# Kernel tuning notes

Measured on AMD Instinct MI355X. Metric: run time of the kernel, lower is better.

Reference implementation:

```python
import jax, jax.numpy as jnp
import numpy as np

N_NODES = 50000
N_EDGES = 300000
D = 256
N_RELS = 500


def setup_inputs() -> dict:
    key = jax.random.key(0)
    ks = jax.random.split(key, 12)
    s = 1.0 / np.sqrt(D)  # keep activations O(1) through the dense transforms
    return {
        "h": jax.random.normal(ks[0], (N_NODES, D), dtype=jnp.float32),
        "prev_h": jax.random.normal(ks[1], (N_NODES, D), dtype=jnp.float32),
        "emb_rel": jax.random.normal(ks[2], (N_RELS, D), dtype=jnp.float32),
        "norm": jax.random.uniform(ks[3], (N_NODES, 1), dtype=jnp.float32),
        "weight_neighbor": jax.random.normal(ks[4], (D, D), dtype=jnp.float32) * s,
        "loop_weight": jax.random.normal(ks[5], (D, D), dtype=jnp.float32) * s,
        "evolve_loop_weight": jax.random.normal(ks[6], (D, D), dtype=jnp.float32) * s,
        "skip_connect_weight": jax.random.normal(ks[7], (D, D), dtype=jnp.float32) * s,
        "skip_connect_bias": jnp.zeros((D,), dtype=jnp.float32),
        "src": jax.random.randint(ks[8], (N_EDGES,), 0, N_NODES),
        "dst": jax.random.randint(ks[9], (N_EDGES,), 0, N_NODES),
        "etype": jax.random.randint(ks[10], (N_EDGES,), 0, N_RELS),
    }


def reference(h, prev_h, emb_rel, norm, weight_neighbor, loop_weight,
              evolve_loop_weight, skip_connect_weight, skip_connect_bias,
              src, dst, etype):
    n_nodes = h.shape[0]
    # msg_func: per-edge gather of src features + relation embedding, dense transform
    msg = (h[src] + emb_rel[etype]) @ weight_neighbor          # [E, D]
    # fn.sum: segment-sum messages into destination nodes
    agg = jax.ops.segment_sum(msg, dst, num_segments=n_nodes)  # [N, D]
    # apply_func: multiply by per-node norm
    agg = agg * norm
    # self-loop: loop_weight where in_degree > 0, evolve_loop_weight otherwise
    in_deg = jax.ops.segment_sum(jnp.ones_like(dst), dst, num_segments=n_nodes)
    has_in = (in_deg > 0)[:, None]
    loop_message = jnp.where(has_in, h @ loop_weight, h @ evolve_loop_weight)
    # skip connection gate
    skip_weight = jax.nn.sigmoid(prev_h @ skip_connect_weight + skip_connect_bias)
    node_repr = skip_weight * (agg + loop_message) + (1.0 - skip_weight) * prev_h
    return jax.nn.relu(node_repr)
```

## Files before the change

### kernel.cpp

```cpp
#include <hip/hip_runtime.h>
#include <cstdint>
#include <cstddef>

#define N_NODES 50000
#define N_EDGES 300000
#define DIM     256
#define KTOT    768
#define N_RELS  500
#define XW      768

#define SCAN_BLK  256
#define SCAN_NBLK ((N_NODES + SCAN_BLK - 1) / SCAN_BLK)

#define CONV_ELEMS ((2 * N_NODES + N_RELS) * DIM)
#define CONV_BLKS  ((CONV_ELEMS / 8 + 255) / 256)
#define HIST_BLKS  ((N_EDGES + 255) / 256)

typedef unsigned short u16;
typedef __attribute__((ext_vector_type(8))) short short8v;
typedef __attribute__((ext_vector_type(4))) float float4v;

static __device__ __forceinline__ u16 f2bf(float f) {
    union { float f; unsigned u; } v; v.f = f;
    unsigned u = v.u;
    unsigned r = u + 0x7FFFu + ((u >> 16) & 1u);
    return (u16)(r >> 16);
}
static __device__ __forceinline__ float bf2f(u16 b) {
    union { unsigned u; float f; } v; v.u = ((unsigned)b) << 16; return v.f;
}

static __device__ __forceinline__ void gld16(const void* g, u16* l) {
    __builtin_amdgcn_global_load_lds(
        (const __attribute__((address_space(1))) unsigned int*)g,
        (__attribute__((address_space(3))) unsigned int*)l,
        16, 0, 0);
}

__global__ void prep_kernel(const float* __restrict__ h, const float* __restrict__ prev_h,
                            const float* __restrict__ emb,
                            const float* __restrict__ Wn, const float* __restrict__ Wl,
                            const float* __restrict__ Wsc, const int* __restrict__ dstv,
                            u16* __restrict__ Xcat, u16* __restrict__ embb,
                            u16* __restrict__ Wt, int* __restrict__ deg) {
    int b = blockIdx.x;
    if (b < CONV_BLKS) {
        int i = b * 256 + threadIdx.x;
        int e0 = i * 8;
        if (e0 >= CONV_ELEMS) return;
        const float* s; u16* d;
        if (e0 < N_NODES * DIM) {
            int n = e0 >> 8, c = e0 & 255;
            s = h + e0; d = Xcat + (size_t)n * XW + 256 + c;
        } else if (e0 < 2 * N_NODES * DIM) {
            int o = e0 - N_NODES * DIM;
            int n = o >> 8, c = o & 255;
            s = prev_h + o; d = Xcat + (size_t)n * XW + 512 + c;
        } else {
            int o = e0 - 2 * N_NODES * DIM;
            s = emb + o; d = embb + o;
        }
        float4 a = *(const float4*)(s);
        float4 c2 = *(const float4*)(s + 4);
        u16 o8[8] = { f2bf(a.x), f2bf(a.y), f2bf(a.z), f2bf(a.w),
                      f2bf(c2.x), f2bf(c2.y), f2bf(c2.z), f2bf(c2.w) };
        *(uint4*)d = *(const uint4*)o8;
    } else if (b < CONV_BLKS + KTOT) {
        int k = b - CONV_BLKS;
        int dd = threadIdx.x;
        const float* W = (k < 256) ? Wn : ((k < 512) ? Wl : Wsc);
        Wt[(size_t)dd * KTOT + k] = f2bf(W[(k & 255) * DIM + dd]);
    } else {
        int e = (b - CONV_BLKS - KTOT) * 256 + threadIdx.x;
        if (e < N_EDGES) atomicAdd(&deg[dstv[e]], 1);
    }
}

__global__ void scanA_kernel(const int* __restrict__ deg, int* __restrict__ excl_local,
                             int* __restrict__ block_sum) {
    __shared__ int sdata[SCAN_BLK];
    int t = threadIdx.x, i = blockIdx.x * SCAN_BLK + t;
    int v = (i < N_NODES) ? deg[i] : 0;
    sdata[t] = v;
    __syncthreads();
    for (int off = 1; off < SCAN_BLK; off <<= 1) {
        int u = (t >= off) ? sdata[t - off] : 0;
        __syncthreads();
        sdata[t] += u;
        __syncthreads();
    }
    if (i < N_NODES) excl_local[i] = sdata[t] - v;
    if (t == SCAN_BLK - 1) block_sum[blockIdx.x] = sdata[t];
}

__global__ void scanB_kernel(const int* __restrict__ block_sum, int* __restrict__ block_base,
                             int* __restrict__ offsets) {
    __shared__ int sdata[SCAN_NBLK];
    int t = threadIdx.x;
    int v = (t < SCAN_NBLK) ? block_sum[t] : 0;
    if (t < SCAN_NBLK) sdata[t] = v;
    __syncthreads();
    for (int off = 1; off < SCAN_NBLK; off <<= 1) {
        int u = (t >= off && t < SCAN_NBLK) ? sdata[t - off] : 0;
        __syncthreads();
        if (t < SCAN_NBLK) sdata[t] += u;
        __syncthreads();
    }
    if (t < SCAN_NBLK) block_base[t] = sdata[t] - v;
    if (t == SCAN_NBLK - 1) offsets[N_NODES] = sdata[t];
}

__global__ void scanC_kernel(const int* __restrict__ excl_local, const int* __restrict__ block_base,
                             int* __restrict__ offsets, int* __restrict__ cursor) {
    int i = blockIdx.x * SCAN_BLK + threadIdx.x;
    if (i < N_NODES) {
        int e = block_base[blockIdx.x] + excl_local[i];
        offsets[i] = e; cursor[i] = e;
    }
}

__global__ void scatter_kernel(const int* __restrict__ src, const int* __restrict__ dstv,
                               const int* __restrict__ et, int* __restrict__ cursor,
                               unsigned* __restrict__ esee) {
    int e = blockIdx.x * 256 + threadIdx.x;
    if (e >= N_EDGES) return;
    int d = dstv[e];
    int pos = atomicAdd(&cursor[d], 1);
    esee[pos] = (unsigned)src[e] * N_RELS + (unsigned)et[e];
}

__global__ void agg_kernel(u16* __restrict__ Xcat, const u16* __restrict__ embb,
                           const float* __restrict__ norm, const int* __restrict__ offsets,
                           const unsigned* __restrict__ esee,
                           int* __restrict__ wl_count, int* __restrict__ wl) {
    int wave = (blockIdx.x * 256 + threadIdx.x) >> 6;
    int lane = threadIdx.x & 63;
    if (wave >= N_NODES) return;
    int n = wave;
    int s0 = offsets[n], s1 = offsets[n + 1];
    int c4 = lane * 4;
    float4 acc = make_float4(0.f, 0.f, 0.f, 0.f);
    int e = s0;
    for (; e + 3 < s1; e += 4) {
        unsigned v0 = esee[e], v1 = esee[e + 1], v2 = esee[e + 2], v3 = esee[e + 3];
        unsigned sa = v0 / N_RELS, ta = v0 - sa * N_RELS;
        unsigned sb = v1 / N_RELS, tb = v1 - sb * N_RELS;
        unsigned sc = v2 / N_RELS, tc = v2 - sc * N_RELS;
        unsigned sd = v3 / N_RELS, td = v3 - sd * N_RELS;
        ushort4 ha = *(const ushort4*)(Xcat + (size_t)sa * XW + 256 + c4);
        ushort4 ea = *(const ushort4*)(embb + (size_t)ta * DIM + c4);
        ushort4 hb = *(const ushort4*)(Xcat + (size_t)sb * XW + 256 + c4);
        ushort4 eb = *(const ushort4*)(embb + (size_t)tb * DIM + c4);
        ushort4 hc = *(const ushort4*)(Xcat + (size_t)sc * XW + 256 + c4);
        ushort4 ec = *(const ushort4*)(embb + (size_t)tc * DIM + c4);
        ushort4 hd = *(const ushort4*)(Xcat + (size_t)sd * XW + 256 + c4);
        ushort4 ed = *(const ushort4*)(embb + (size_t)td * DIM + c4);
        acc.x += (bf2f(ha.x) + bf2f(ea.x)) + (bf2f(hb.x) + bf2f(eb.x))
               + (bf2f(hc.x) + bf2f(ec.x)) + (bf2f(hd.x) + bf2f(ed.x));
        acc.y += (bf2f(ha.y) + bf2f(ea.y)) + (bf2f(hb.y) + bf2f(eb.y))
               + (bf2f(hc.y) + bf2f(ec.y)) + (bf2f(hd.y) + bf2f(ed.y));
        acc.z += (bf2f(ha.z) + bf2f(ea.z)) + (bf2f(hb.z) + bf2f(eb.z))
               + (bf2f(hc.z) + bf2f(ec.z)) + (bf2f(hd.z) + bf2f(ed.z));
        acc.w += (bf2f(ha.w) + bf2f(ea.w)) + (bf2f(hb.w) + bf2f(eb.w))
               + (bf2f(hc.w) + bf2f(ec.w)) + (bf2f(hd.w) + bf2f(ed.w));
    }
    for (; e < s1; e++) {
        unsigned v = esee[e];
        unsigned s = v / N_RELS;
        unsigned t = v - s * N_RELS;
        ushort4 hv = *(const ushort4*)(Xcat + (size_t)s * XW + 256 + c4);
        ushort4 ev = *(const ushort4*)(embb + (size_t)t * DIM + c4);
        acc.x += bf2f(hv.x) + bf2f(ev.x);
        acc.y += bf2f(hv.y) + bf2f(ev.y);
        acc.z += bf2f(hv.z) + bf2f(ev.z);
        acc.w += bf2f(hv.w) + bf2f(ev.w);
    }
    float nr = norm[n];
    u16 o[4] = { f2bf(acc.x * nr), f2bf(acc.y * nr), f2bf(acc.z * nr), f2bf(acc.w * nr) };
    *(ushort4*)(Xcat + (size_t)n * XW + c4) = *(const ushort4*)o;
    if (lane == 0 && s1 == s0) { int idx = atomicAdd(wl_count, 1); wl[idx] = n; }
}

__launch_bounds__(512, 4)
__global__ void gemm_kernel(const u16* __restrict__ Xcat, const u16* __restrict__ Wt,
                            const float* __restrict__ prev_h, const float* __restrict__ bias,
                            float* __restrict__ out) {
    __shared__ __align__(16) u16 lds[40960];
    int tid  = threadIdx.x;
    int wave = tid >> 6, lane = tid & 63, q = lane >> 4, m16 = lane & 15;
    int wm = wave >> 2;
    int wnn = (wave & 3) * 64;
    int m0 = blockIdx.x * 64;
    int lr = lane >> 3, lc8 = lane & 7;
    int sc8 = (lc8 ^ lr) << 3;

    int arow = wave * 8 + lr;
    int ga = (m0 + arow < N_NODES) ? (m0 + arow) : (N_NODES - 1);
    const u16* sA = Xcat + (size_t)ga * XW + sc8;
    const u16* sB = Wt + (size_t)(wave * 32 + lr) * KTOT + sc8;

    float4v acc1[2][4], acc2[2][4];
#pragma unroll
    for (int i = 0; i < 2; i++)
#pragma unroll
        for (int j = 0; j < 4; j++) { acc1[i][j] = (float4v)0.f; acc2[i][j] = (float4v)0.f; }

    auto stage = [&](int kt, int buf) {
#pragma unroll
        for (int j = 0; j < 4; j++)
            gld16(sB + (size_t)j * 8 * KTOT + kt * 64,
                  &lds[8192 + buf * 16384 + wave * 2048 + j * 512]);
        gld16(sA + kt * 64, &lds[buf * 4096 + wave * 512]);
    };

    stage(0, 0);
    stage(1, 1);

    int sw = (m16 & 7) << 3;

#pragma unroll
    for (int kt = 0; kt < 12; kt++) {
        int buf = kt & 1;
        if (kt < 11) asm volatile("s_waitcnt vmcnt(5)" ::: "memory");
        else         asm volatile("s_waitcnt vmcnt(0)" ::: "memory");
        __builtin_amdgcn_sched_barrier(0);
        __builtin_amdgcn_s_barrier();
        __builtin_amdgcn_sched_barrier(0);

#pragma unroll
        for (int kk = 0; kk < 2; kk++) {
            int ck = (kk * 32 + q * 8) ^ sw;
            short8v af[2], bfr[4];
#pragma unroll
            for (int mi = 0; mi < 2; mi++)
                af[mi] = *(const short8v*)(&lds[buf * 4096 + (wm * 32 + mi * 16 + m16) * 64 + ck]);
#pragma unroll
            for (int ni = 0; ni < 4; ni++)
                bfr[ni] = *(const short8v*)(&lds[8192 + buf * 16384 + (wnn + ni * 16 + m16) * 64 + ck]);
            if (kt < 8) {
#pragma unroll
                for (int mi = 0; mi < 2; mi++)
#pragma unroll
                    for (int ni = 0; ni < 4; ni++)
                        acc1[mi][ni] = __builtin_amdgcn_mfma_f32_16x16x32_bf16(
                            af[mi], bfr[ni], acc1[mi][ni], 0, 0, 0);
            } else {
#pragma unroll
                for (int mi = 0; mi < 2; mi++)
#pragma unroll
                    for (int ni = 0; ni < 4; ni++)
                        acc2[mi][ni] = __builtin_amdgcn_mfma_f32_16x16x32_bf16(
                            af[mi], bfr[ni], acc2[mi][ni], 0, 0, 0);
            }
        }

        __builtin_amdgcn_sched_barrier(0);
        __builtin_amdgcn_s_barrier();
        __builtin_amdgcn_sched_barrier(0);
        if (kt + 2 < 12) stage(kt + 2, buf);
    }

#pragma unroll
    for (int mi = 0; mi < 2; mi++) {
#pragma unroll
        for (int ni = 0; ni < 4; ni++) {
            int d = wnn + ni * 16 + m16;
            float b = bias[d];
#pragma unroll
            for (int r = 0; r < 4; r++) {
                int node = m0 + wm * 32 + mi * 16 + q * 4 + r;
                if (node < N_NODES) {
                    float S  = acc2[mi][ni][r] + b;
                    float sg = 1.f / (1.f + __expf(-S));
                    float ph = prev_h[(size_t)node * DIM + d];
                    float v  = sg * acc1[mi][ni][r] + (1.f - sg) * ph;
                    out[(size_t)node * DIM + d] = fmaxf(v, 0.f);
                }
            }
        }
    }
}

__global__ void fixup_kernel(const float* __restrict__ h, const float* __restrict__ prev_h,
                             const float* __restrict__ We, const float* __restrict__ Wsc,
                             const float* __restrict__ bias, const int* __restrict__ wl_count,
                             const int* __restrict__ wl, float* __restrict__ out) {
    __shared__ float ph[DIM], hh[DIM];
    int d = threadIdx.x;
    int cnt = *wl_count;
    for (int i = blockIdx.x; i < cnt; i += gridDim.x) {
        int n = wl[i];
        ph[d] = prev_h[(size_t)n * DIM + d];
        hh[d] = h[(size_t)n * DIM + d];
        __syncthreads();
        float s = 0.f, l = 0.f;
        for (int k = 0; k < DIM; k++) {
            s += ph[k] * Wsc[k * DIM + d];
            l += hh[k] * We[k * DIM + d];
        }
        float sg = 1.f / (1.f + __expf(-(s + bias[d])));
        float v = sg * l + (1.f - sg) * ph[d];
        out[(size_t)n * DIM + d] = fmaxf(v, 0.f);
        __syncthreads();
    }
}

extern "C" void kernel_launch(void* const* d_in, const int* in_sizes, int n_in,
                              void* d_out, int out_size, void* d_ws, size_t ws_size,
                              hipStream_t stream) {
    const float* h      = (const float*)d_in[0];
    const float* prev_h = (const float*)d_in[1];
    const float* emb    = (const float*)d_in[2];
    const float* norm   = (const float*)d_in[3];
    const float* Wn     = (const float*)d_in[4];
    const float* Wl     = (const float*)d_in[5];
    const float* We     = (const float*)d_in[6];
    const float* Wsc    = (const float*)d_in[7];
    const float* bias   = (const float*)d_in[8];
    const int*   src    = (const int*)d_in[9];
    const int*   dstv   = (const int*)d_in[10];
    const int*   et     = (const int*)d_in[11];
    float* out = (float*)d_out;

    char* ws = (char*)d_ws;
    size_t off = 0;
    auto alloc = [&](size_t bytes) -> char* {
        char* p = ws + off; off += (bytes + 255) & ~(size_t)255; return p;
    };
    u16* Xcat    = (u16*)alloc((size_t)N_NODES * XW * 2);
    u16* embb    = (u16*)alloc((size_t)N_RELS * DIM * 2);
    u16* Wt      = (u16*)alloc((size_t)DIM * KTOT * 2);
    int* deg     = (int*)alloc((size_t)N_NODES * 4);
    int* wlcnt   = (int*)alloc(16);
    int* wl      = (int*)alloc((size_t)N_NODES * 4);
    int* offsets = (int*)alloc((size_t)(N_NODES + 1) * 4);
    int* cursor  = (int*)alloc((size_t)N_NODES * 4);
    unsigned* esee = (unsigned*)alloc((size_t)N_EDGES * 4);
    int* excl    = (int*)alloc((size_t)N_NODES * 4);
    int* bsum    = (int*)alloc((size_t)SCAN_NBLK * 4);
    int* bbase   = (int*)alloc((size_t)SCAN_NBLK * 4);

    hipMemsetAsync(deg, 0, (size_t)N_NODES * 4, stream);
    hipMemsetAsync(wlcnt, 0, 4, stream);

    prep_kernel<<<CONV_BLKS + KTOT + HIST_BLKS, 256, 0, stream>>>(
        h, prev_h, emb, Wn, Wl, Wsc, dstv, Xcat, embb, Wt, deg);
    scanA_kernel<<<SCAN_NBLK, SCAN_BLK, 0, stream>>>(deg, excl, bsum);
    scanB_kernel<<<1, SCAN_BLK, 0, stream>>>(bsum, bbase, offsets);
    scanC_kernel<<<SCAN_NBLK, SCAN_BLK, 0, stream>>>(excl, bbase, offsets, cursor);
    scatter_kernel<<<(N_EDGES + 255) / 256, 256, 0, stream>>>(src, dstv, et, cursor, esee);
    agg_kernel<<<(N_NODES + 3) / 4, 256, 0, stream>>>(Xcat, embb, norm, offsets, esee, wlcnt, wl);
    gemm_kernel<<<(N_NODES + 63) / 64, 512, 0, stream>>>(Xcat, Wt, prev_h, bias, out);
    fixup_kernel<<<256, 256, 0, stream>>>(h, prev_h, We, Wsc, bias, wlcnt, wl, out);
}
```

Before: 312.7 us.

## Split concatenated activation buffer into three arrays and convert prev_h in agg

Replaces the interleaved 768-wide bf16 Xcat row layout with three separate 256-wide arrays (aggregate, h, prev_h), and moves the prev_h bf16 conversion from the prep kernel into the aggregation kernel. The h gather in aggregation then reads from a compact, denser array, which should improve cache locality, and the prep kernel does less work. The GEMM picks the source array per K-tile. In exchange the aggregation kernel carries extra prev_h load and store traffic.

After: 316.9 us. About the same (+1.3%).

```diff
diff --git a/kernel.cpp b/kernel.cpp
--- a/kernel.cpp
+++ b/kernel.cpp
@@ -7,12 +7,11 @@
 #define DIM     256
 #define KTOT    768
 #define N_RELS  500
-#define XW      768
 
 #define SCAN_BLK  256
 #define SCAN_NBLK ((N_NODES + SCAN_BLK - 1) / SCAN_BLK)
 
-#define CONV_ELEMS ((2 * N_NODES + N_RELS) * DIM)
+#define CONV_ELEMS ((N_NODES + N_RELS) * DIM)
 #define CONV_BLKS  ((CONV_ELEMS / 8 + 255) / 256)
 #define HIST_BLKS  ((N_EDGES + 255) / 256)
 
@@ -37,11 +36,10 @@
         16, 0, 0);
 }
 
-__global__ void prep_kernel(const float* __restrict__ h, const float* __restrict__ prev_h,
-                            const float* __restrict__ emb,
+__global__ void prep_kernel(const float* __restrict__ h, const float* __restrict__ emb,
                             const float* __restrict__ Wn, const float* __restrict__ Wl,
                             const float* __restrict__ Wsc, const int* __restrict__ dstv,
-                            u16* __restrict__ Xcat, u16* __restrict__ embb,
+                            u16* __restrict__ Xh, u16* __restrict__ embb,
                             u16* __restrict__ Wt, int* __restrict__ deg) {
     int b = blockIdx.x;
     if (b < CONV_BLKS) {
@@ -49,17 +47,8 @@
         int e0 = i * 8;
         if (e0 >= CONV_ELEMS) return;
         const float* s; u16* d;
-        if (e0 < N_NODES * DIM) {
-            int n = e0 >> 8, c = e0 & 255;
-            s = h + e0; d = Xcat + (size_t)n * XW + 256 + c;
-        } else if (e0 < 2 * N_NODES * DIM) {
-            int o = e0 - N_NODES * DIM;
-            int n = o >> 8, c = o & 255;
-            s = prev_h + o; d = Xcat + (size_t)n * XW + 512 + c;
-        } else {
-            int o = e0 - 2 * N_NODES * DIM;
-            s = emb + o; d = embb + o;
-        }
+        if (e0 < N_NODES * DIM) { s = h + e0; d = Xh + e0; }
+        else { int o = e0 - N_NODES * DIM; s = emb + o; d = embb + o; }
         float4 a = *(const float4*)(s);
         float4 c2 = *(const float4*)(s + 4);
         u16 o8[8] = { f2bf(a.x), f2bf(a.y), f2bf(a.z), f2bf(a.w),
@@ -129,9 +118,10 @@
     esee[pos] = (unsigned)src[e] * N_RELS + (unsigned)et[e];
 }
 
-__global__ void agg_kernel(u16* __restrict__ Xcat, const u16* __restrict__ embb,
+__global__ void agg_kernel(const u16* __restrict__ Xh, const u16* __restrict__ embb,
                            const float* __restrict__ norm, const int* __restrict__ offsets,
-                           const unsigned* __restrict__ esee,
+                           const unsigned* __restrict__ esee, const float* __restrict__ prev_h,
+                           u16* __restrict__ Xa, u16* __restrict__ Xp,
                            int* __restrict__ wl_count, int* __restrict__ wl) {
     int wave = (blockIdx.x * 256 + threadIdx.x) >> 6;
     int lane = threadIdx.x & 63;
@@ -139,6 +129,7 @@
     int n = wave;
     int s0 = offsets[n], s1 = offsets[n + 1];
     int c4 = lane * 4;
+    float4 pv = *(const float4*)(prev_h + (size_t)n * DIM + c4);
     float4 acc = make_float4(0.f, 0.f, 0.f, 0.f);
     int e = s0;
     for (; e + 3 < s1; e += 4) {
@@ -147,13 +138,13 @@
         unsigned sb = v1 / N_RELS, tb = v1 - sb * N_RELS;
         unsigned sc = v2 / N_RELS, tc = v2 - sc * N_RELS;
         unsigned sd = v3 / N_RELS, td = v3 - sd * N_RELS;
-        ushort4 ha = *(const ushort4*)(Xcat + (size_t)sa * XW + 256 + c4);
+        ushort4 ha = *(const ushort4*)(Xh + (size_t)sa * DIM + c4);
         ushort4 ea = *(const ushort4*)(embb + (size_t)ta * DIM + c4);
-        ushort4 hb = *(const ushort4*)(Xcat + (size_t)sb * XW + 256 + c4);
+        ushort4 hb = *(const ushort4*)(Xh + (size_t)sb * DIM + c4);
         ushort4 eb = *(const ushort4*)(embb + (size_t)tb * DIM + c4);
-        ushort4 hc = *(const ushort4*)(Xcat + (size_t)sc * XW + 256 + c4);
+        ushort4 hc = *(const ushort4*)(Xh + (size_t)sc * DIM + c4);
         ushort4 ec = *(const ushort4*)(embb + (size_t)tc * DIM + c4);
-        ushort4 hd = *(const ushort4*)(Xcat + (size_t)sd * XW + 256 + c4);
+        ushort4 hd = *(const ushort4*)(Xh + (size_t)sd * DIM + c4);
         ushort4 ed = *(const ushort4*)(embb + (size_t)td * DIM + c4);
         acc.x += (bf2f(ha.x) + bf2f(ea.x)) + (bf2f(hb.x) + bf2f(eb.x))
                + (bf2f(hc.x) + bf2f(ec.x)) + (bf2f(hd.x) + bf2f(ed.x));
@@ -168,7 +159,7 @@
         unsigned v = esee[e];
         unsigned s = v / N_RELS;
         unsigned t = v - s * N_RELS;
-        ushort4 hv = *(const ushort4*)(Xcat + (size_t)s * XW + 256 + c4);
+        ushort4 hv = *(const ushort4*)(Xh + (size_t)s * DIM + c4);
         ushort4 ev = *(const ushort4*)(embb + (size_t)t * DIM + c4);
         acc.x += bf2f(hv.x) + bf2f(ev.x);
         acc.y += bf2f(hv.y) + bf2f(ev.y);
@@ -177,12 +168,15 @@
     }
     float nr = norm[n];
     u16 o[4] = { f2bf(acc.x * nr), f2bf(acc.y * nr), f2bf(acc.z * nr), f2bf(acc.w * nr) };
-    *(ushort4*)(Xcat + (size_t)n * XW + c4) = *(const ushort4*)o;
+    *(ushort4*)(Xa + (size_t)n * DIM + c4) = *(const ushort4*)o;
+    u16 p4[4] = { f2bf(pv.x), f2bf(pv.y), f2bf(pv.z), f2bf(pv.w) };
+    *(ushort4*)(Xp + (size_t)n * DIM + c4) = *(const ushort4*)p4;
     if (lane == 0 && s1 == s0) { int idx = atomicAdd(wl_count, 1); wl[idx] = n; }
 }
 
 __launch_bounds__(512, 4)
-__global__ void gemm_kernel(const u16* __restrict__ Xcat, const u16* __restrict__ Wt,
+__global__ void gemm_kernel(const u16* __restrict__ Xa, const u16* __restrict__ Xh,
+                            const u16* __restrict__ Xp, const u16* __restrict__ Wt,
                             const float* __restrict__ prev_h, const float* __restrict__ bias,
                             float* __restrict__ out) {
     __shared__ __align__(16) u16 lds[40960];
@@ -196,7 +190,9 @@
 
     int arow = wave * 8 + lr;
     int ga = (m0 + arow < N_NODES) ? (m0 + arow) : (N_NODES - 1);
-    const u16* sA = Xcat + (size_t)ga * XW + sc8;
+    const u16* sAa = Xa + (size_t)ga * DIM + sc8;
+    const u16* sAh = Xh + (size_t)ga * DIM + sc8;
+    const u16* sAp = Xp + (size_t)ga * DIM + sc8;
     const u16* sB = Wt + (size_t)(wave * 32 + lr) * KTOT + sc8;
 
     float4v acc1[2][4], acc2[2][4];
@@ -210,7 +206,8 @@
         for (int j = 0; j < 4; j++)
             gld16(sB + (size_t)j * 8 * KTOT + kt * 64,
                   &lds[8192 + buf * 16384 + wave * 2048 + j * 512]);
-        gld16(sA + kt * 64, &lds[buf * 4096 + wave * 512]);
+        const u16* base = (kt < 4) ? sAa : ((kt < 8) ? sAh : sAp);
+        gld16(base + (kt & 3) * 64, &lds[buf * 4096 + wave * 512]);
     };
 
     stage(0, 0);
@@ -327,7 +324,9 @@
     auto alloc = [&](size_t bytes) -> char* {
         char* p = ws + off; off += (bytes + 255) & ~(size_t)255; return p;
     };
-    u16* Xcat    = (u16*)alloc((size_t)N_NODES * XW * 2);
+    u16* Xa      = (u16*)alloc((size_t)N_NODES * DIM * 2);
+    u16* Xh      = (u16*)alloc((size_t)N_NODES * DIM * 2);
+    u16* Xp      = (u16*)alloc((size_t)N_NODES * DIM * 2);
     u16* embb    = (u16*)alloc((size_t)N_RELS * DIM * 2);
     u16* Wt      = (u16*)alloc((size_t)DIM * KTOT * 2);
     int* deg     = (int*)alloc((size_t)N_NODES * 4);
@@ -344,12 +343,13 @@
     hipMemsetAsync(wlcnt, 0, 4, stream);
 
     prep_kernel<<<CONV_BLKS + KTOT + HIST_BLKS, 256, 0, stream>>>(
-        h, prev_h, emb, Wn, Wl, Wsc, dstv, Xcat, embb, Wt, deg);
+        h, emb, Wn, Wl, Wsc, dstv, Xh, embb, Wt, deg);
     scanA_kernel<<<SCAN_NBLK, SCAN_BLK, 0, stream>>>(deg, excl, bsum);
     scanB_kernel<<<1, SCAN_BLK, 0, stream>>>(bsum, bbase, offsets);
     scanC_kernel<<<SCAN_NBLK, SCAN_BLK, 0, stream>>>(excl, bbase, offsets, cursor);
     scatter_kernel<<<(N_EDGES + 255) / 256, 256, 0, stream>>>(src, dstv, et, cursor, esee);
-    agg_kernel<<<(N_NODES + 3) / 4, 256, 0, stream>>>(Xcat, embb, norm, offsets, esee, wlcnt, wl);
-    gemm_kernel<<<(N_NODES + 63) / 64, 512, 0, stream>>>(Xcat, Wt, prev_h, bias, out);
+    agg_kernel<<<(N_NODES + 3) / 4, 256, 0, stream>>>(Xh, embb, norm, offsets, esee, prev_h,
+                                                      Xa, Xp, wlcnt, wl);
+    gemm_kernel<<<(N_NODES + 63) / 64, 512, 0, stream>>>(Xa, Xh, Xp, Wt, prev_h, bias, out);
     fixup_kernel<<<256, 256, 0, stream>>>(h, prev_h, We, Wsc, bias, wlcnt, wl, out);
 }
```
